# Kernel optimization log

Measured on AMD Instinct MI355X. Metric: run time of the kernel, lower is better.

The kernel has to match this reference:

```python
import jax, jax.numpy as jnp
import numpy as np

INPUT_SIZE = 512
LABEL_NUM = 8
OUTPUT_SIZE = 64
H1 = 1024  # shared bottom width
H2 = 512   # expert hidden width
B = 8192


def setup_inputs() -> dict:
    key = jax.random.key(0)
    ks = jax.random.split(key, 8)
    s_in = 1.0 / np.sqrt(INPUT_SIZE)
    s_h1 = 1.0 / np.sqrt(H1)
    s_h2 = 1.0 / np.sqrt(H2)
    return {
        "input": jax.random.normal(ks[0], (B, INPUT_SIZE), dtype=jnp.float32),
        "category": jax.random.randint(ks[1], (B,), 0, LABEL_NUM, dtype=jnp.int32),
        # shared bottom Linear(input_size, 1024): stored as [in, out]
        "W_in": jax.random.uniform(ks[2], (INPUT_SIZE, H1), jnp.float32, -s_in, s_in),
        "b_in": jax.random.uniform(ks[3], (H1,), jnp.float32, -s_in, s_in),
        # per-expert Linear(1024, 512) stacked over experts
        "W1": jax.random.uniform(ks[4], (LABEL_NUM, H1, H2), jnp.float32, -s_h1, s_h1),
        "b1": jax.random.uniform(ks[5], (LABEL_NUM, H2), jnp.float32, -s_h1, s_h1),
        # per-expert Linear(512, output_size) stacked over experts
        "W2": jax.random.uniform(ks[6], (LABEL_NUM, H2, OUTPUT_SIZE), jnp.float32, -s_h2, s_h2),
        "b2": jax.random.uniform(ks[7], (LABEL_NUM, OUTPUT_SIZE), jnp.float32, -s_h2, s_h2),
    }


def reference(input, category, W_in, b_in, W1, b1, W2, b2):
    # Shared bottom: Linear + ELU -> [B, H1]
    mid = jax.nn.elu(input @ W_in + b_in)
    # Run all experts densely, then hard-select per-sample expert output.
    # (Faithful to per-sample hard routing; small expert count makes this clean.)
    h = jax.nn.elu(jnp.einsum("bd,edh->beh", mid, W1) + b1[None, :, :])  # [B,E,H2]
    out_all = jnp.einsum("beh,eho->beo", h, W2) + b2[None, :, :]          # [B,E,O]
    # gather the chosen expert's output for each sample
    out = jnp.take_along_axis(out_all, category[:, None, None].astype(jnp.int32).repeat(1, axis=1), axis=1)
    return out[:, 0, :]  # [B, O]
```

## Files before the change

### kernel.cpp

```cpp
#include <hip/hip_runtime.h>

typedef unsigned short u16;
typedef __bf16 bf16x8 __attribute__((ext_vector_type(8)));
typedef float f32x4 __attribute__((ext_vector_type(4)));

#define GLD_LDS(gptr, lptr) \
  __builtin_amdgcn_global_load_lds((const __attribute__((address_space(1))) void*)(gptr), \
                                   (__attribute__((address_space(3))) void*)(lptr), 16, 0, 0)

__device__ __forceinline__ u16 f2b(float f) {
  union { __bf16 h; u16 u; } v; v.h = (__bf16)f; return v.u;
}
__device__ __forceinline__ float elu1(float v) {
  return v > 0.f ? v : (__expf(v) - 1.f);
}

__device__ void hist_body(int rb, const int* __restrict__ cat, int* __restrict__ cnts) {
  __shared__ int c8[8];
  const int tid = threadIdx.x;
  if (tid < 8) c8[tid] = 0;
  __syncthreads();
  if (tid < 128) atomicAdd(&c8[cat[rb * 128 + tid]], 1);
  __syncthreads();
  if (tid < 8) cnts[rb * 8 + tid] = c8[tid];
}

__device__ void scatter_body(int rb, const int* __restrict__ cat,
                             const int* __restrict__ cnts,
                             int* __restrict__ list, int* __restrict__ off) {
  __shared__ int lc[512];
  __shared__ int lcur[8];
  __shared__ int starts[8];
  const int tid = threadIdx.x;
  lc[tid] = cnts[tid];
  lc[tid + 256] = cnts[tid + 256];
  if (tid < 8) lcur[tid] = 0;
  __syncthreads();
  if (tid < 8) {
    const int c = tid;
    int base = 0;
    for (int cc = 0; cc < c; cc++) {
      int s = 0;
      for (int b = 0; b < 64; b++) s += lc[b * 8 + cc];
      base += s;
    }
    int pre = 0;
    for (int b = 0; b < rb; b++) pre += lc[b * 8 + c];
    starts[c] = base + pre;
    if (rb == 0) {
      off[c] = base;
      if (c == 7) {
        int s = 0;
        for (int b = 0; b < 64; b++) s += lc[b * 8 + 7];
        off[8] = base + s;
      }
    }
  }
  __syncthreads();
  if (tid < 128) {
    const int idx = rb * 128 + tid;
    const int c = cat[idx];
    const int r = atomicAdd(&lcur[c], 1);
    list[starts[c] + r] = idx;
  }
}

__global__ __launch_bounds__(256) void wcvt(const float* __restrict__ W_in,
                                            const float* __restrict__ W1,
                                            const float* __restrict__ W2,
                                            const float* __restrict__ x,
                                            const int* __restrict__ cat,
                                            u16* __restrict__ o0, u16* __restrict__ o1,
                                            u16* __restrict__ o2, u16* __restrict__ ox,
                                            int* __restrict__ cnts) {
  const int bid = blockIdx.x, tid = threadIdx.x;
  if (bid >= 3264) {
    hist_body(bid - 3264, cat, cnts);
    return;
  }
  if (bid >= 1216) {
    const size_t base = (size_t)(bid - 1216) * 2048 + (size_t)tid * 8;
    float4 v0 = *reinterpret_cast<const float4*>(x + base);
    float4 v1 = *reinterpret_cast<const float4*>(x + base + 4);
    ushort4 a, b;
    a.x = f2b(v0.x); a.y = f2b(v0.y); a.z = f2b(v0.z); a.w = f2b(v0.w);
    b.x = f2b(v1.x); b.y = f2b(v1.y); b.z = f2b(v1.z); b.w = f2b(v1.w);
    *reinterpret_cast<ushort4*>(ox + base) = a;
    *reinterpret_cast<ushort4*>(ox + base + 4) = b;
    return;
  }
  const float* src; u16* dst; int R, C, tr, tc; size_t zoff;
  if (bid < 128) {
    src = W_in; dst = o0; R = 512; C = 1024; tr = bid >> 4; tc = bid & 15; zoff = 0;
  } else if (bid < 1152) {
    int t = bid - 128; int z = t >> 7, rem = t & 127;
    src = W1; dst = o1; R = 1024; C = 512; tr = rem >> 3; tc = rem & 7;
    zoff = (size_t)z * R * C;
  } else {
    int t = bid - 1152; int z = t >> 3;
    src = W2; dst = o2; R = 512; C = 64; tr = t & 7; tc = 0;
    zoff = (size_t)z * R * C;
  }
  __shared__ float tbuf[64][65];
  const float* sp = src + zoff + (size_t)(tr * 64) * C + tc * 64;
#pragma unroll
  for (int i = 0; i < 4; i++) {
    const int rr = (tid >> 4) + i * 16, f = tid & 15;
    float4 v = *reinterpret_cast<const float4*>(sp + (size_t)rr * C + f * 4);
    tbuf[rr][f * 4 + 0] = v.x; tbuf[rr][f * 4 + 1] = v.y;
    tbuf[rr][f * 4 + 2] = v.z; tbuf[rr][f * 4 + 3] = v.w;
  }
  __syncthreads();
  u16* dp = dst + zoff + (size_t)(tc * 64) * R + tr * 64;
#pragma unroll
  for (int i = 0; i < 4; i++) {
    const int u = tid + i * 256;
    const int c = u >> 4, rq = u & 15;
    ushort4 w;
    w.x = f2b(tbuf[rq * 4 + 0][c]); w.y = f2b(tbuf[rq * 4 + 1][c]);
    w.z = f2b(tbuf[rq * 4 + 2][c]); w.w = f2b(tbuf[rq * 4 + 3][c]);
    *reinterpret_cast<ushort4*>(dp + (size_t)c * R + rq * 4) = w;
  }
}


template<int LAYER, int BN, int K, int N>
__global__ __launch_bounds__(256, 4) void gemm_t(
    const u16* __restrict__ A, const u16* __restrict__ Bw,
    const float* __restrict__ bias,
    const int* __restrict__ list, const int* __restrict__ off,
    u16* __restrict__ outb, float* __restrict__ outf,
    const int* __restrict__ cat, const int* __restrict__ cnts,
    int* __restrict__ wlist, int* __restrict__ woff) {
  __shared__ alignas(16) u16 As[2][64 * 32];
  __shared__ alignas(16) u16 Bs[2][BN * 32];

  if constexpr (LAYER == 1) {
    if (blockIdx.y == 8) {
      if (blockIdx.x < 64) scatter_body(blockIdx.x, cat, cnts, wlist, woff);
      return;
    }
  }

  const int tid = threadIdx.x;
  const int wave = tid >> 6, lane = tid & 63;

  int e = 0, start = 0, cnt = 0, rowbase;
  if constexpr (LAYER == 1) {
    rowbase = blockIdx.x * 64;
  } else {
    int t = blockIdx.x;
    int found = -1;
    for (e = 0; e < 8; e++) {
      int tiles = (off[e + 1] - off[e] + 63) >> 6;
      if (t < tiles) { found = e; break; }
      t -= tiles;
    }
    if (found < 0) return;
    start = off[e];
    cnt = off[e + 1] - start;
    rowbase = t * 64;
  }
  const int col0 = blockIdx.y * BN;

  const int srow = tid >> 2, skc = tid & 3;
  const int kxs = (skc ^ (srow & 3)) * 8;

  const u16* a_src;
  if constexpr (LAYER == 1) {
    a_src = A + (size_t)(rowbase + srow) * K + kxs;
  } else if constexpr (LAYER == 2) {
    int gr = list[start + min(rowbase + srow, cnt - 1)];
    a_src = A + (size_t)gr * K + kxs;
  } else {
    a_src = A + (size_t)(start + min(rowbase + srow, cnt - 1)) * K + kxs;
  }
  const u16* Bbase = Bw + (LAYER == 1 ? (size_t)0 : (size_t)e * N * K);
  const u16* b_src0 = Bbase + (size_t)(col0 + srow) * K + kxs;
  const u16* b_src1 = Bbase + (size_t)(col0 + 64 + srow) * K + kxs;

  const int wbase = wave * 512;

  constexpr int NR = BN / 32;
  const int wy = wave & 1, wx = wave >> 1;
  const int fr = lane & 15, kg = lane >> 4;
  const int kx = (kg ^ (fr & 3)) * 8;
  const int ar0 = (wy * 32 + fr) * 32 + kx;
  const int br0 = (wx * (BN / 2) + fr) * 32 + kx;

  f32x4 acc[2][NR] = {};

  constexpr int NK = K / 32;
  GLD_LDS(a_src, &As[0][wbase]);
  GLD_LDS(b_src0, &Bs[0][wbase]);
  if constexpr (BN == 128) GLD_LDS(b_src1, &Bs[0][2048 + wbase]);
  __syncthreads();
  for (int it = 0; it < NK; ++it) {
    const int cur = it & 1;
    if (it + 1 < NK) {
      const int nxt = cur ^ 1;
      const int kt = (it + 1) * 32;
      GLD_LDS(a_src + kt, &As[nxt][wbase]);
      GLD_LDS(b_src0 + kt, &Bs[nxt][wbase]);
      if constexpr (BN == 128) GLD_LDS(b_src1 + kt, &Bs[nxt][2048 + wbase]);
    }
    bf16x8 af[2], bfv[NR];
#pragma unroll
    for (int m = 0; m < 2; m++) af[m] = *(const bf16x8*)&As[cur][ar0 + m * 16 * 32];
#pragma unroll
    for (int n = 0; n < NR; n++) bfv[n] = *(const bf16x8*)&Bs[cur][br0 + n * 16 * 32];
#pragma unroll
    for (int m = 0; m < 2; m++)
#pragma unroll
      for (int n = 0; n < NR; n++)
        acc[m][n] = __builtin_amdgcn_mfma_f32_16x16x32_bf16(af[m], bfv[n], acc[m][n], 0, 0, 0);
    __syncthreads();
  }

#pragma unroll
  for (int n = 0; n < NR; n++) {
    const int col = col0 + wx * (BN / 2) + n * 16 + fr;
    const float bc = bias[(LAYER == 1 ? 0 : e * N) + col];
#pragma unroll
    for (int m = 0; m < 2; m++) {
      const int rloc = wy * 32 + m * 16 + kg * 4;
#pragma unroll
      for (int j = 0; j < 4; j++) {
        const float v = acc[m][n][j] + bc;
        if constexpr (LAYER == 1) {
          outb[(size_t)(rowbase + rloc + j) * N + col] = f2b(elu1(v));
        } else if constexpr (LAYER == 2) {
          const int slot = rowbase + rloc + j;
          if (slot < cnt) outb[(size_t)(start + slot) * N + col] = f2b(elu1(v));
        } else {
          const int slot = rowbase + rloc + j;
          if (slot < cnt) outf[(size_t)list[start + slot] * N + col] = v;
        }
      }
    }
  }
}


extern "C" void kernel_launch(void* const* d_in, const int* in_sizes, int n_in,
                              void* d_out, int out_size, void* d_ws, size_t ws_size,
                              hipStream_t stream) {
  const float* x    = (const float*)d_in[0];
  const int*   cat  = (const int*)d_in[1];
  const float* W_in = (const float*)d_in[2];
  const float* b_in = (const float*)d_in[3];
  const float* W1   = (const float*)d_in[4];
  const float* b1   = (const float*)d_in[5];
  const float* W2   = (const float*)d_in[6];
  const float* b2   = (const float*)d_in[7];
  float* out = (float*)d_out;

  char* p = (char*)d_ws;
  u16* xb   = (u16*)p; p += (size_t)8192 * 512 * 2;
  u16* midb = (u16*)p; p += (size_t)8192 * 1024 * 2;
  u16* hb   = (u16*)p; p += (size_t)8192 * 512 * 2;
  u16* wtin = (u16*)p; p += (size_t)1024 * 512 * 2;
  u16* w1t  = (u16*)p; p += (size_t)8 * 512 * 1024 * 2;
  u16* w2t  = (u16*)p; p += (size_t)8 * 64 * 512 * 2;
  int* list = (int*)p; p += (size_t)8192 * 4;
  int* off  = (int*)p; p += 64;
  int* cnts = (int*)p; p += 64 * 8 * 4;

  wcvt<<<3328, 256, 0, stream>>>(W_in, W1, W2, x, cat, wtin, w1t, w2t, xb, cnts);

  gemm_t<1, 128, 512, 1024><<<dim3(128, 9), 256, 0, stream>>>(
      xb, wtin, b_in, nullptr, nullptr, midb, nullptr, cat, cnts, list, off);
  gemm_t<2, 128, 1024, 512><<<dim3(136, 4), 256, 0, stream>>>(
      midb, w1t, b1, list, off, hb, nullptr, nullptr, nullptr, nullptr, nullptr);
  gemm_t<3, 64, 512, 64><<<dim3(136, 1), 256, 0, stream>>>(
      hb, w2t, b2, list, off, nullptr, out, nullptr, nullptr, nullptr, nullptr);
}
```

Baseline: 70.58 us.

## Fuse input bf16 conversion into layer-1 GEMM and overlap expert weight transposes

The separate fp32→bf16 conversion of the input activations is removed. The layer-1 GEMM now loads fp32 rows into registers, converts them, and writes them to LDS, so the bf16 copy of x is never written to or read from global memory. The W1/W2 transpose-convert blocks move out of the prologue kernel into extra grid rows of the layer-1 GEMM launch, so they run alongside the first GEMM instead of before it. In exchange, the A operand goes through registers instead of direct global-to-LDS loads, which adds VGPR pressure and LDS store work to the GEMM main loop, and the LDS is shared through a union.

```diff
diff --git a/kernel.cpp b/kernel.cpp
--- a/kernel.cpp
+++ b/kernel.cpp
@@ -1,6 +1,7 @@
 #include <hip/hip_runtime.h>
 
 typedef unsigned short u16;
+typedef unsigned int u32;
 typedef __bf16 bf16x8 __attribute__((ext_vector_type(8)));
 typedef float f32x4 __attribute__((ext_vector_type(4)));
 
@@ -13,6 +14,31 @@
 }
 __device__ __forceinline__ float elu1(float v) {
   return v > 0.f ? v : (__expf(v) - 1.f);
+}
+
+__device__ void transpose_tile(float (*tbuf)[65], const float* __restrict__ src,
+                               u16* __restrict__ dst, int R, int C, int tr, int tc,
+                               size_t zoff) {
+  const int tid = threadIdx.x;
+  const float* sp = src + zoff + (size_t)(tr * 64) * C + tc * 64;
+#pragma unroll
+  for (int i = 0; i < 4; i++) {
+    const int rr = (tid >> 4) + i * 16, f = tid & 15;
+    float4 v = *reinterpret_cast<const float4*>(sp + (size_t)rr * C + f * 4);
+    tbuf[rr][f * 4 + 0] = v.x; tbuf[rr][f * 4 + 1] = v.y;
+    tbuf[rr][f * 4 + 2] = v.z; tbuf[rr][f * 4 + 3] = v.w;
+  }
+  __syncthreads();
+  u16* dp = dst + zoff + (size_t)(tc * 64) * R + tr * 64;
+#pragma unroll
+  for (int i = 0; i < 4; i++) {
+    const int u = tid + i * 256;
+    const int c = u >> 4, rq = u & 15;
+    ushort4 w;
+    w.x = f2b(tbuf[rq * 4 + 0][c]); w.y = f2b(tbuf[rq * 4 + 1][c]);
+    w.z = f2b(tbuf[rq * 4 + 2][c]); w.w = f2b(tbuf[rq * 4 + 3][c]);
+    *reinterpret_cast<ushort4*>(dp + (size_t)c * R + rq * 4) = w;
+  }
 }
 
 __device__ void hist_body(int rb, const int* __restrict__ cat, int* __restrict__ cnts) {
@@ -65,84 +91,49 @@
   }
 }
 
-__global__ __launch_bounds__(256) void wcvt(const float* __restrict__ W_in,
-                                            const float* __restrict__ W1,
-                                            const float* __restrict__ W2,
-                                            const float* __restrict__ x,
-                                            const int* __restrict__ cat,
-                                            u16* __restrict__ o0, u16* __restrict__ o1,
-                                            u16* __restrict__ o2, u16* __restrict__ ox,
-                                            int* __restrict__ cnts) {
-  const int bid = blockIdx.x, tid = threadIdx.x;
-  if (bid >= 3264) {
-    hist_body(bid - 3264, cat, cnts);
-    return;
-  }
-  if (bid >= 1216) {
-    const size_t base = (size_t)(bid - 1216) * 2048 + (size_t)tid * 8;
-    float4 v0 = *reinterpret_cast<const float4*>(x + base);
-    float4 v1 = *reinterpret_cast<const float4*>(x + base + 4);
-    ushort4 a, b;
-    a.x = f2b(v0.x); a.y = f2b(v0.y); a.z = f2b(v0.z); a.w = f2b(v0.w);
-    b.x = f2b(v1.x); b.y = f2b(v1.y); b.z = f2b(v1.z); b.w = f2b(v1.w);
-    *reinterpret_cast<ushort4*>(ox + base) = a;
-    *reinterpret_cast<ushort4*>(ox + base + 4) = b;
-    return;
-  }
-  const float* src; u16* dst; int R, C, tr, tc; size_t zoff;
-  if (bid < 128) {
-    src = W_in; dst = o0; R = 512; C = 1024; tr = bid >> 4; tc = bid & 15; zoff = 0;
-  } else if (bid < 1152) {
-    int t = bid - 128; int z = t >> 7, rem = t & 127;
-    src = W1; dst = o1; R = 1024; C = 512; tr = rem >> 3; tc = rem & 7;
-    zoff = (size_t)z * R * C;
-  } else {
-    int t = bid - 1152; int z = t >> 3;
-    src = W2; dst = o2; R = 512; C = 64; tr = t & 7; tc = 0;
-    zoff = (size_t)z * R * C;
-  }
+__global__ __launch_bounds__(256) void wsmall(const float* __restrict__ W_in,
+                                              const int* __restrict__ cat,
+                                              u16* __restrict__ o0, int* __restrict__ cnts) {
   __shared__ float tbuf[64][65];
-  const float* sp = src + zoff + (size_t)(tr * 64) * C + tc * 64;
-#pragma unroll
-  for (int i = 0; i < 4; i++) {
-    const int rr = (tid >> 4) + i * 16, f = tid & 15;
-    float4 v = *reinterpret_cast<const float4*>(sp + (size_t)rr * C + f * 4);
-    tbuf[rr][f * 4 + 0] = v.x; tbuf[rr][f * 4 + 1] = v.y;
-    tbuf[rr][f * 4 + 2] = v.z; tbuf[rr][f * 4 + 3] = v.w;
-  }
-  __syncthreads();
-  u16* dp = dst + zoff + (size_t)(tc * 64) * R + tr * 64;
-#pragma unroll
-  for (int i = 0; i < 4; i++) {
-    const int u = tid + i * 256;
-    const int c = u >> 4, rq = u & 15;
-    ushort4 w;
-    w.x = f2b(tbuf[rq * 4 + 0][c]); w.y = f2b(tbuf[rq * 4 + 1][c]);
-    w.z = f2b(tbuf[rq * 4 + 2][c]); w.w = f2b(tbuf[rq * 4 + 3][c]);
-    *reinterpret_cast<ushort4*>(dp + (size_t)c * R + rq * 4) = w;
-  }
+  if (blockIdx.x >= 128) { hist_body(blockIdx.x - 128, cat, cnts); return; }
+  transpose_tile(tbuf, W_in, o0, 512, 1024, blockIdx.x >> 4, blockIdx.x & 15, 0);
 }
 
 
 template<int LAYER, int BN, int K, int N>
 __global__ __launch_bounds__(256, 4) void gemm_t(
-    const u16* __restrict__ A, const u16* __restrict__ Bw,
-    const float* __restrict__ bias,
+    const float* __restrict__ Xf, const u16* __restrict__ A,
+    const u16* __restrict__ Bw, const float* __restrict__ bias,
     const int* __restrict__ list, const int* __restrict__ off,
     u16* __restrict__ outb, float* __restrict__ outf,
     const int* __restrict__ cat, const int* __restrict__ cnts,
-    int* __restrict__ wlist, int* __restrict__ woff) {
-  __shared__ alignas(16) u16 As[2][64 * 32];
-  __shared__ alignas(16) u16 Bs[2][BN * 32];
+    int* __restrict__ wlist, int* __restrict__ woff,
+    const float* __restrict__ Wc1, const float* __restrict__ Wc2,
+    u16* __restrict__ o1, u16* __restrict__ o2) {
+  struct GBuf { alignas(16) u16 As[2][2048]; alignas(16) u16 Bs[2][BN * 32]; };
+  __shared__ union SM { GBuf g; float tbuf[64][65]; } sm;
+
+  const int tid = threadIdx.x;
 
   if constexpr (LAYER == 1) {
     if (blockIdx.y == 8) {
       if (blockIdx.x < 64) scatter_body(blockIdx.x, cat, cnts, wlist, woff);
       return;
     }
-  }
-
-  const int tid = threadIdx.x;
+    if (blockIdx.y >= 9) {
+      if (blockIdx.y <= 16) {
+        const int t = (blockIdx.y - 9) * 128 + blockIdx.x;
+        const int z = t >> 7, rem = t & 127;
+        transpose_tile(sm.tbuf, Wc1, o1, 1024, 512, rem >> 3, rem & 7,
+                       (size_t)z * 1024 * 512);
+      } else if (blockIdx.x < 64) {
+        const int t = blockIdx.x, z = t >> 3;
+        transpose_tile(sm.tbuf, Wc2, o2, 512, 64, t & 7, 0, (size_t)z * 512 * 64);
+      }
+      return;
+    }
+  }
+
   const int wave = tid >> 6, lane = tid & 63;
 
   int e = 0, start = 0, cnt = 0, rowbase;
@@ -166,9 +157,10 @@
   const int srow = tid >> 2, skc = tid & 3;
   const int kxs = (skc ^ (srow & 3)) * 8;
 
-  const u16* a_src;
+  const float* ax = nullptr;
+  const u16* a_src = nullptr;
   if constexpr (LAYER == 1) {
-    a_src = A + (size_t)(rowbase + srow) * K + kxs;
+    ax = Xf + (size_t)(rowbase + srow) * K + kxs;
   } else if constexpr (LAYER == 2) {
     int gr = list[start + min(rowbase + srow, cnt - 1)];
     a_src = A + (size_t)gr * K + kxs;
@@ -190,30 +182,52 @@
 
   f32x4 acc[2][NR] = {};
 
+  float4 va0, va1;
+  auto LOAD_A1 = [&](int t) {
+    va0 = *reinterpret_cast<const float4*>(ax + t * 32);
+    va1 = *reinterpret_cast<const float4*>(ax + t * 32 + 4);
+  };
+  auto WRITE_A1 = [&](int buf) {
+    uint4 w;
+    w.x = (u32)f2b(va0.x) | ((u32)f2b(va0.y) << 16);
+    w.y = (u32)f2b(va0.z) | ((u32)f2b(va0.w) << 16);
+    w.z = (u32)f2b(va1.x) | ((u32)f2b(va1.y) << 16);
+    w.w = (u32)f2b(va1.z) | ((u32)f2b(va1.w) << 16);
+    *reinterpret_cast<uint4*>(&sm.g.As[buf][srow * 32 + skc * 8]) = w;
+  };
+  auto COMPUTE = [&](int buf) {
+    bf16x8 af[2], bfv[NR];
+#pragma unroll
+    for (int m = 0; m < 2; m++) af[m] = *(const bf16x8*)&sm.g.As[buf][ar0 + m * 16 * 32];
+#pragma unroll
+    for (int n = 0; n < NR; n++) bfv[n] = *(const bf16x8*)&sm.g.Bs[buf][br0 + n * 16 * 32];
+#pragma unroll
+    for (int m = 0; m < 2; m++)
+#pragma unroll
+      for (int n = 0; n < NR; n++)
+        acc[m][n] = __builtin_amdgcn_mfma_f32_16x16x32_bf16(af[m], bfv[n], acc[m][n], 0, 0, 0);
+  };
+
   constexpr int NK = K / 32;
-  GLD_LDS(a_src, &As[0][wbase]);
-  GLD_LDS(b_src0, &Bs[0][wbase]);
-  if constexpr (BN == 128) GLD_LDS(b_src1, &Bs[0][2048 + wbase]);
-  __syncthreads();
+  if constexpr (LAYER == 1) LOAD_A1(0);
+  else GLD_LDS(a_src, &sm.g.As[0][wbase]);
+  GLD_LDS(b_src0, &sm.g.Bs[0][wbase]);
+  if constexpr (BN == 128) GLD_LDS(b_src1, &sm.g.Bs[0][2048 + wbase]);
+  if constexpr (LAYER == 1) WRITE_A1(0);
+  __syncthreads();
+
   for (int it = 0; it < NK; ++it) {
     const int cur = it & 1;
+    const int nxt = cur ^ 1;
     if (it + 1 < NK) {
-      const int nxt = cur ^ 1;
       const int kt = (it + 1) * 32;
-      GLD_LDS(a_src + kt, &As[nxt][wbase]);
-      GLD_LDS(b_src0 + kt, &Bs[nxt][wbase]);
-      if constexpr (BN == 128) GLD_LDS(b_src1 + kt, &Bs[nxt][2048 + wbase]);
-    }
-    bf16x8 af[2], bfv[NR];
-#pragma unroll
-    for (int m = 0; m < 2; m++) af[m] = *(const bf16x8*)&As[cur][ar0 + m * 16 * 32];
-#pragma unroll
-    for (int n = 0; n < NR; n++) bfv[n] = *(const bf16x8*)&Bs[cur][br0 + n * 16 * 32];
-#pragma unroll
-    for (int m = 0; m < 2; m++)
-#pragma unroll
-      for (int n = 0; n < NR; n++)
-        acc[m][n] = __builtin_amdgcn_mfma_f32_16x16x32_bf16(af[m], bfv[n], acc[m][n], 0, 0, 0);
+      if constexpr (LAYER == 1) LOAD_A1(it + 1);
+      else GLD_LDS(a_src + kt, &sm.g.As[nxt][wbase]);
+      GLD_LDS(b_src0 + kt, &sm.g.Bs[nxt][wbase]);
+      if constexpr (BN == 128) GLD_LDS(b_src1 + kt, &sm.g.Bs[nxt][2048 + wbase]);
+    }
+    COMPUTE(cur);
+    if constexpr (LAYER == 1) { if (it + 1 < NK) WRITE_A1(nxt); }
     __syncthreads();
   }
 
@@ -256,7 +270,6 @@
   float* out = (float*)d_out;
 
   char* p = (char*)d_ws;
-  u16* xb   = (u16*)p; p += (size_t)8192 * 512 * 2;
   u16* midb = (u16*)p; p += (size_t)8192 * 1024 * 2;
   u16* hb   = (u16*)p; p += (size_t)8192 * 512 * 2;
   u16* wtin = (u16*)p; p += (size_t)1024 * 512 * 2;
@@ -266,12 +279,17 @@
   int* off  = (int*)p; p += 64;
   int* cnts = (int*)p; p += 64 * 8 * 4;
 
-  wcvt<<<3328, 256, 0, stream>>>(W_in, W1, W2, x, cat, wtin, w1t, w2t, xb, cnts);
-
-  gemm_t<1, 128, 512, 1024><<<dim3(128, 9), 256, 0, stream>>>(
-      xb, wtin, b_in, nullptr, nullptr, midb, nullptr, cat, cnts, list, off);
+  wsmall<<<192, 256, 0, stream>>>(W_in, cat, wtin, cnts);
+
+  gemm_t<1, 128, 512, 1024><<<dim3(128, 18), 256, 0, stream>>>(
+      x, nullptr, wtin, b_in, nullptr, nullptr, midb, nullptr,
+      cat, cnts, list, off, W1, W2, w1t, w2t);
+
   gemm_t<2, 128, 1024, 512><<<dim3(136, 4), 256, 0, stream>>>(
-      midb, w1t, b1, list, off, hb, nullptr, nullptr, nullptr, nullptr, nullptr);
+      nullptr, midb, w1t, b1, list, off, hb, nullptr,
+      nullptr, nullptr, nullptr, nullptr, nullptr, nullptr, nullptr, nullptr);
+
   gemm_t<3, 64, 512, 64><<<dim3(136, 1), 256, 0, stream>>>(
-      hb, w2t, b2, list, off, nullptr, out, nullptr, nullptr, nullptr, nullptr);
-}
+      nullptr, hb, w2t, b2, list, off, nullptr, out,
+      nullptr, nullptr, nullptr, nullptr, nullptr, nullptr, nullptr, nullptr);
+}
```

Result: faster. 66.82 us (-5.3%).
